# Performance work log

Measured on AMD Instinct MI355X. Metric: run time of the kernel, lower is better.

The kernel has to match this reference:

```python
import jax, jax.numpy as jnp
import numpy as np

_EPS = 1e-5
_NH, _DH = 4, 64  # heads, dim_head


def _ln(x, g, b):
    m = x.mean(-1, keepdims=True)
    v = ((x - m) ** 2).mean(-1, keepdims=True)
    return (x - m) / jnp.sqrt(v + _EPS) * g + b


def _leaky(x):
    return jnp.where(x > 0, x, 0.01 * x)


def _bn_eval(x, g, b):
    # eval-mode BatchNorm with running_mean=0, running_var=1
    return x * (g / np.sqrt(1.0 + _EPS)) + b


def setup_inputs() -> dict:
    key = jax.random.key(0)
    ks = jax.random.split(key, 20)
    B, L, S, D, T, H = 4096, 8, 877, 256, 137, 128
    f = jnp.float32

    def rn(k, shape, s=0.02):
        return jax.random.normal(k, shape, dtype=f) * s

    inp = {}
    inp['source'] = jax.random.normal(ks[0], (B, S), dtype=f)
    inp['source_neighbor'] = jax.random.normal(ks[1], (B, L, S), dtype=f)
    inp['cell_inf'] = jax.random.uniform(ks[2], (B, L + 1, 13), dtype=f)
    # encoder_rna: 877 -> 512 -> 256, Linear+BN(eval)+LeakyReLU
    inp['enc_w1'] = rn(ks[3], (S, 512)); inp['enc_b1'] = jnp.zeros((512,), f)
    inp['enc_bn1_g'] = jnp.ones((512,), f); inp['enc_bn1_b'] = jnp.zeros((512,), f)
    inp['enc_w2'] = rn(ks[4], (512, D)); inp['enc_b2'] = jnp.zeros((D,), f)
    inp['enc_bn2_g'] = jnp.ones((D,), f); inp['enc_bn2_b'] = jnp.zeros((D,), f)
    # projection_rna: Linear(256,256) + LayerNorm + ReLU
    inp['proj_w'] = rn(ks[5], (D, D)); inp['proj_b'] = jnp.zeros((D,), f)
    inp['proj_ln_g'] = jnp.ones((D,), f); inp['proj_ln_b'] = jnp.zeros((D,), f)
    # 1-layer pre-norm transformer (4 heads, dim_head 64, ff_mult 2)
    inp['attn_ln_g'] = jnp.ones((D,), f); inp['attn_ln_b'] = jnp.zeros((D,), f)
    inp['wq'] = rn(ks[6], (D, D)); inp['wk'] = rn(ks[7], (D, D)); inp['wv'] = rn(ks[8], (D, D))
    inp['wo'] = rn(ks[9], (D, D)); inp['wo_b'] = jnp.zeros((D,), f)
    inp['ff_ln_g'] = jnp.ones((D,), f); inp['ff_ln_b'] = jnp.zeros((D,), f)
    inp['ff_w1'] = rn(ks[10], (D, 2 * D)); inp['ff_b1'] = jnp.zeros((2 * D,), f)
    inp['ff_w2'] = rn(ks[11], (2 * D, D)); inp['ff_b2'] = jnp.zeros((D,), f)
    # learned tokens
    inp['token_center'] = rn(ks[12], (1, 1, D))
    inp['token_neigh_1'] = rn(ks[13], (1, 1, D))
    inp['token_neigh_2'] = rn(ks[14], (1, 1, D))
    inp['cell_tokens'] = rn(ks[15], (1, 1, 13, D))
    # 137 independent predict heads, batched: Linear(256,128)+BN+LeakyReLU+Linear(128,1,no bias)
    inp['pred_w1'] = rn(ks[16], (T, D, H)); inp['pred_b1'] = jnp.zeros((T, H), f)
    inp['pred_bn_g'] = jnp.ones((T, H), f); inp['pred_bn_b'] = jnp.zeros((T, H), f)
    inp['pred_w2'] = rn(ks[17], (T, H))
    return inp


def _forward(source, source_neighbor, cell_inf, enc_w1, enc_b1, enc_bn1_g, enc_bn1_b,
             enc_w2, enc_b2, enc_bn2_g, enc_bn2_b, proj_w, proj_b, proj_ln_g, proj_ln_b,
             attn_ln_g, attn_ln_b, wq, wk, wv, wo, wo_b, ff_ln_g, ff_ln_b,
             ff_w1, ff_b1, ff_w2, ff_b2, token_center, token_neigh_1, token_neigh_2,
             cell_tokens, pred_w1, pred_b1, pred_bn_g, pred_bn_b, pred_w2):
    B = source.shape[0]
    x = jnp.concatenate([source[:, None, :], source_neighbor], axis=1)  # [B,N,877]
    N = x.shape[1]
    l = N - 1
    half = l // 2
    valid = jnp.abs(x).sum(-1) > 0                      # [B,N] bool
    vm = valid.astype(x.dtype)[..., None]               # [B,N,1]
    D = token_center.shape[-1]
    # role tokens: center / first-half neigh / second-half neigh, masked
    role = jnp.concatenate([
        token_center,
        jnp.broadcast_to(token_neigh_1, (1, half, D)),
        jnp.broadcast_to(token_neigh_2, (1, l - half, D)),
    ], axis=1) * vm                                      # [B,N,D]
    # class tokens: weighted sum over 13 cell-type tokens, masked
    class_tok = (cell_tokens * cell_inf[..., None]).sum(-2) * vm  # [B,N,D]
    # encoder_rna (dropouts are eval identity)
    h = _leaky(_bn_eval(x @ enc_w1 + enc_b1, enc_bn1_g, enc_bn1_b))
    h = _leaky(_bn_eval(h @ enc_w2 + enc_b2, enc_bn2_g, enc_bn2_b))  # [B,N,D]
    fo = h + role + class_tok
    fo = jax.nn.relu(_ln(fo @ proj_w + proj_b, proj_ln_g, proj_ln_b))
    # local graph transformer encoder (depth=1, pre-norm, masked attention)
    hn = _ln(fo, attn_ln_g, attn_ln_b)
    q = (hn @ wq).reshape(B, N, _NH, _DH)
    k = (hn @ wk).reshape(B, N, _NH, _DH)
    v = (hn @ wv).reshape(B, N, _NH, _DH)
    scores = jnp.einsum('bihd,bjhd->bhij', q, k) * (_DH ** -0.5)
    scores = jnp.where(valid[:, None, None, :], scores, -1e9)
    attn = jax.nn.softmax(scores, axis=-1)
    o = jnp.einsum('bhij,bjhd->bihd', attn, v).reshape(B, N, _NH * _DH)
    fo = fo + o @ wo + wo_b
    hn2 = _ln(fo, ff_ln_g, ff_ln_b)
    fo = fo + jax.nn.gelu(hn2 @ ff_w1 + ff_b1) @ ff_w2 + ff_b2
    feat = fo[:, 0, :]                                   # [B,D] center token
    # 137 predict heads as one batched GEMM + fused BN/LeakyReLU
    ph = jnp.einsum('bd,tdh->bth', feat, pred_w1) + pred_b1   # [B,137,128]
    ph = _leaky(_bn_eval(ph, pred_bn_g, pred_bn_b))
    out = jnp.einsum('bth,th->bt', ph, pred_w2)               # [B,137]
    return out


def reference(source, source_neighbor, cell_inf, enc_w1, enc_b1, enc_bn1_g, enc_bn1_b,
              enc_w2, enc_b2, enc_bn2_g, enc_bn2_b, proj_w, proj_b, proj_ln_g, proj_ln_b,
              attn_ln_g, attn_ln_b, wq, wk, wv, wo, wo_b, ff_ln_g, ff_ln_b,
              ff_w1, ff_b1, ff_w2, ff_b2, token_center, token_neigh_1, token_neigh_2,
              cell_tokens, pred_w1, pred_b1, pred_bn_g, pred_bn_b, pred_w2):
    return _forward(source, source_neighbor, cell_inf, enc_w1, enc_b1, enc_bn1_g, enc_bn1_b,
                    enc_w2, enc_b2, enc_bn2_g, enc_bn2_b, proj_w, proj_b, proj_ln_g, proj_ln_b,
                    attn_ln_g, attn_ln_b, wq, wk, wv, wo, wo_b, ff_ln_g, ff_ln_b,
                    ff_w1, ff_b1, ff_w2, ff_b2, token_center, token_neigh_1, token_neigh_2,
                    cell_tokens, pred_w1, pred_b1, pred_bn_g, pred_bn_b, pred_w2)
```

## Files before the change

### kernel.cpp

```cpp
#include <hip/hip_runtime.h>
#include <hip/hip_bf16.h>
#include <math.h>

typedef __hip_bfloat16 bf16;
typedef __attribute__((ext_vector_type(8))) short short8;
typedef __attribute__((ext_vector_type(4))) float f32x4;

#define BB 4096
#define LL 8
#define NN 9
#define SS 877
#define DD 256
#define D2 512
#define TT 137
#define HH 128
#define MM (BB*NN)
#define KP1 896

__device__ __forceinline__ float lrelu(float x){ return x > 0.f ? x : 0.01f*x; }
__device__ __forceinline__ float gelu_tanh(float x){
    float x3 = x*x*x;
    float t = tanhf(0.7978845608028654f*(x + 0.044715f*x3));
    return 0.5f*x*(1.f + t);
}
__device__ __forceinline__ short f2b(float x){
    union { bf16 h; short s; } u; u.h = __float2bfloat16(x); return u.s;
}
__device__ __forceinline__ float b2f(bf16 v){ return __bfloat162float(v); }

struct SwzD { const float* src; unsigned short* dst; int K; int N; int NB; long long base; };
struct SwzTab { SwzD d[10]; long long total; };

__global__ __launch_bounds__(256) void k_swzall(SwzTab tab){
    for (long long f0 = (long long)blockIdx.x*256 + threadIdx.x; f0 < tab.total;
         f0 += (long long)gridDim.x*256){
        int di = 0;
        #pragma unroll
        for (int q = 1; q < 10; q++) if (f0 >= tab.d[q].base) di = q;
        const SwzD dd = tab.d[di];
        long long f = f0 - dd.base;
        int j = (int)(f & 7); int lane = (int)((f>>3)&63); int h = (int)((f>>9)&7);
        long long u = f>>12;
        int nb = (int)(u % dd.NB), kb = (int)(u / dd.NB);
        int k = kb*32 + ((lane>>4)<<3) + j;
        int n = nb*128 + h*16 + (lane&15);
        float v = (k < dd.K) ? dd.src[(size_t)k*dd.N + n] : 0.f;
        dd.dst[f] = (unsigned short)f2b(v);
    }
}

__global__ __launch_bounds__(256) void k_prep(const float* __restrict__ src,
                                              const float* __restrict__ srcn,
                                              float* __restrict__ vm,
                                              unsigned short* __restrict__ xbf){
    int m = blockIdx.x; int b = m / NN, n = m % NN;
    const float* row = (n == 0) ? src + (size_t)b*SS
                                : srcn + ((size_t)b*LL + (n-1))*SS;
    unsigned short* orow = xbf + (size_t)m*KP1;
    float s = 0.f;
    for (int i = threadIdx.x; i < KP1; i += 256){
        float v = (i < SS) ? row[i] : 0.f;
        s += fabsf(v);
        orow[i] = (unsigned short)f2b(v);
    }
    #pragma unroll
    for (int o = 32; o > 0; o >>= 1) s += __shfl_xor(s, o);
    __shared__ float part[4];
    if ((threadIdx.x & 63) == 0) part[threadIdx.x>>6] = s;
    __syncthreads();
    if (threadIdx.x == 0)
        vm[m] = ((part[0]+part[1]+part[2]+part[3]) > 0.f) ? 1.f : 0.f;
}

#define EPI_NONE 0
#define EPI_BN_LEAKY 1
#define EPI_RES 2
#define EPI_GELU 3

__global__ __launch_bounds__(256) void k_mgemm(
    const unsigned short* __restrict__ A, int lda,
    const unsigned short* __restrict__ Wsw, int NB, int nKb,
    const float* __restrict__ bias, const float* __restrict__ bng,
    const float* __restrict__ bnb, const float* __restrict__ res,
    int res_stride, int mode,
    float* __restrict__ out, bf16* __restrict__ outbf, int ldo)
{
    __shared__ short8 As[512];
    int row0 = blockIdx.x*128;
    int nb = blockIdx.y;
    int tid = threadIdx.x;
    int wv = tid>>6, lane = tid&63;
    int wr = wv>>1, wc = wv&1;
    int quad = lane>>4, l15 = lane&15;

    f32x4 zz = {0.f,0.f,0.f,0.f};
    f32x4 acc[4][4];
    #pragma unroll
    for (int i=0;i<4;i++){ acc[i][0]=zz; acc[i][1]=zz; acc[i][2]=zz; acc[i][3]=zz; }

    int m0 = tid>>2, k8 = tid&3;
    int m1 = m0 + 64;
    int dst0 = (m0>>4)*64 + (m0&15) + (k8<<4);
    int dst1 = (m1>>4)*64 + (m1&15) + (k8<<4);
    const short8* W8 = (const short8*)Wsw;

    for (int kb = 0; kb < nKb; kb++){
        int k0 = kb*32;
        uint4 v0 = *(const uint4*)(A + (size_t)(row0+m0)*lda + k0 + k8*8);
        uint4 v1 = *(const uint4*)(A + (size_t)(row0+m1)*lda + k0 + k8*8);
        short8 bfr[4];
        #pragma unroll
        for (int h = 0; h < 4; h++)
            bfr[h] = W8[((size_t)(kb*NB + nb)*8 + wc*4 + h)*64 + lane];
        __syncthreads();
        ((uint4*)As)[dst0] = v0;
        ((uint4*)As)[dst1] = v1;
        __syncthreads();
        #pragma unroll
        for (int i = 0; i < 4; i++){
            short8 af = As[(wr*4+i)*64 + lane];
            #pragma unroll
            for (int h = 0; h < 4; h++)
                acc[i][h] = __builtin_amdgcn_mfma_f32_16x16x32_bf16(af, bfr[h], acc[i][h], 0,0,0);
        }
    }

    const float inv = rsqrtf(1.f + 1e-5f);
    #pragma unroll
    for (int i = 0; i < 4; i++){
        int rbase = row0 + wr*64 + i*16 + quad*4;
        #pragma unroll
        for (int h = 0; h < 4; h++){
            int c = nb*128 + wc*64 + h*16 + l15;
            float bi = bias ? bias[c] : 0.f;
            #pragma unroll
            for (int reg = 0; reg < 4; reg++){
                int r = rbase + reg;
                float y = acc[i][h][reg] + bi;
                if (mode == EPI_BN_LEAKY)      y = lrelu(y*(bng[c]*inv) + bnb[c]);
                else if (mode == EPI_RES)      y += res[(size_t)r*res_stride + c];
                else if (mode == EPI_GELU)     y = gelu_tanh(y);
                if (out)   out[(size_t)r*ldo + c] = y;
                if (outbf) outbf[(size_t)r*ldo + c] = __float2bfloat16(y);
            }
        }
    }
}

__global__ __launch_bounds__(256) void k_pred_mfma(
    const unsigned short* __restrict__ feat,
    const unsigned short* __restrict__ Wsw,
    const float* __restrict__ b1, const float* __restrict__ bg,
    const float* __restrict__ bb, const float* __restrict__ w2,
    float* __restrict__ outp)
{
    __shared__ short8 As[512];
    int row0 = blockIdx.x*128;
    int t = blockIdx.y;
    int tid = threadIdx.x;
    int wv = tid>>6, lane = tid&63;
    int quad = lane>>4, l15 = lane&15;

    const float inv = rsqrtf(1.f + 1e-5f);
    float b1v[8], bgv[8], bbv[8], w2v[8];
    #pragma unroll
    for (int h = 0; h < 8; h++){
        int hc = t*HH + h*16 + l15;
        b1v[h] = b1[hc]; bgv[h] = bg[hc]*inv; bbv[h] = bb[hc]; w2v[h] = w2[hc];
    }

    f32x4 zz = {0.f,0.f,0.f,0.f};
    f32x4 acc[2][8];
    #pragma unroll
    for (int i=0;i<2;i++)
        #pragma unroll
        for (int h=0;h<8;h++) acc[i][h] = zz;

    int m0 = tid>>2, k8 = tid&3;
    int m1 = m0 + 64;
    int dst0 = (m0>>4)*64 + (m0&15) + (k8<<4);
    int dst1 = (m1>>4)*64 + (m1&15) + (k8<<4);
    const short8* W8 = (const short8*)Wsw;

    for (int kb = 0; kb < 8; kb++){
        int k0 = kb*32;
        uint4 v0 = *(const uint4*)(feat + (size_t)(row0+m0)*DD + k0 + k8*8);
        uint4 v1 = *(const uint4*)(feat + (size_t)(row0+m1)*DD + k0 + k8*8);
        short8 bfr[8];
        #pragma unroll
        for (int h = 0; h < 8; h++)
            bfr[h] = W8[((size_t)(t*8 + kb)*8 + h)*64 + lane];
        __syncthreads();
        ((uint4*)As)[dst0] = v0;
        ((uint4*)As)[dst1] = v1;
        __syncthreads();
        #pragma unroll
        for (int i = 0; i < 2; i++){
            short8 af = As[(wv*2+i)*64 + lane];
            #pragma unroll
            for (int h = 0; h < 8; h++)
                acc[i][h] = __builtin_amdgcn_mfma_f32_16x16x32_bf16(af, bfr[h], acc[i][h], 0,0,0);
        }
    }

    #pragma unroll
    for (int i = 0; i < 2; i++){
        #pragma unroll
        for (int reg = 0; reg < 4; reg++){
            float p = 0.f;
            #pragma unroll
            for (int h = 0; h < 8; h++){
                float y = (acc[i][h][reg] + b1v[h])*bgv[h] + bbv[h];
                p += lrelu(y) * w2v[h];
            }
            p += __shfl_xor(p, 1);
            p += __shfl_xor(p, 2);
            p += __shfl_xor(p, 4);
            p += __shfl_xor(p, 8);
            if (l15 == 0){
                int r = row0 + wv*32 + i*16 + quad*4 + reg;
                outp[(size_t)r*TT + t] = p;
            }
        }
    }
}

__global__ __launch_bounds__(256) void k_rolecls(const float* __restrict__ tokc,
                                                 const float* __restrict__ tokn1,
                                                 const float* __restrict__ tokn2,
                                                 const float* __restrict__ cell_tokens,
                                                 const float* __restrict__ cell_inf,
                                                 const float* __restrict__ vm,
                                                 float* __restrict__ fo,
                                                 bf16* __restrict__ fobf){
    int m = blockIdx.x, d = threadIdx.x;
    int n = m % NN;
    float v = vm[m];
    const float* role = (n == 0) ? tokc : (n <= 4 ? tokn1 : tokn2);
    float cl = 0.f;
    #pragma unroll
    for (int c = 0; c < 13; c++)
        cl += cell_inf[(size_t)m*13 + c] * cell_tokens[c*DD + d];
    float y = fo[(size_t)m*DD + d] + (role[d] + cl) * v;
    fo[(size_t)m*DD + d] = y;
    fobf[(size_t)m*DD + d] = __float2bfloat16(y);
}

__device__ __forceinline__ float blksum(float v, float* part){
    #pragma unroll
    for (int o = 32; o > 0; o >>= 1) v += __shfl_xor(v, o);
    __syncthreads();
    if ((threadIdx.x & 63) == 0) part[threadIdx.x>>6] = v;
    __syncthreads();
    return part[0]+part[1]+part[2]+part[3];
}

__global__ __launch_bounds__(256) void k_lnchain(const float* __restrict__ in,
                                                 const float* __restrict__ g1, const float* __restrict__ b1,
                                                 const float* __restrict__ g2, const float* __restrict__ b2,
                                                 float* __restrict__ fo1, bf16* __restrict__ hn){
    __shared__ float part[4];
    int m = blockIdx.x, d = threadIdx.x;
    float x = in[(size_t)m*DD + d];
    float mu = blksum(x, part) * (1.f/256.f);
    float dx = x - mu;
    float var = blksum(dx*dx, part) * (1.f/256.f);
    float y = dx * rsqrtf(var + 1e-5f) * g1[d] + b1[d];
    y = fmaxf(y, 0.f);
    fo1[(size_t)m*DD + d] = y;
    float mu2 = blksum(y, part) * (1.f/256.f);
    float dy = y - mu2;
    float var2 = blksum(dy*dy, part) * (1.f/256.f);
    hn[(size_t)m*DD + d] = __float2bfloat16(dy * rsqrtf(var2 + 1e-5f) * g2[d] + b2[d]);
}

__global__ __launch_bounds__(256) void k_ln(const float* __restrict__ in,
                                            const float* __restrict__ g, const float* __restrict__ b,
                                            bf16* __restrict__ out){
    __shared__ float part[4];
    int m = blockIdx.x, d = threadIdx.x;
    float x = in[(size_t)m*DD + d];
    float mu = blksum(x, part) * (1.f/256.f);
    float dx = x - mu;
    float var = blksum(dx*dx, part) * (1.f/256.f);
    out[(size_t)m*DD + d] = __float2bfloat16(dx * rsqrtf(var + 1e-5f) * g[d] + b[d]);
}

__global__ __launch_bounds__(256) void k_attn(const bf16* __restrict__ q,
                                              const bf16* __restrict__ k,
                                              const bf16* __restrict__ v,
                                              const float* __restrict__ vm,
                                              bf16* __restrict__ o){
    int b = blockIdx.x, t = threadIdx.x;
    __shared__ float ks[NN][DD];
    __shared__ float vs[NN][DD];
    __shared__ float qs[DD];
    __shared__ float sc[4][NN];
    __shared__ float val[NN];
    qs[t] = b2f(q[(size_t)b*DD + t]);
    for (int j = 0; j < NN; j++){
        ks[j][t] = b2f(k[((size_t)b*NN + j)*DD + t]);
        vs[j][t] = b2f(v[((size_t)b*NN + j)*DD + t]);
    }
    if (t < NN) val[t] = vm[b*NN + t];
    __syncthreads();
    if (t < 4*NN){
        int h = t / NN, j = t % NN;
        float s = 0.f;
        for (int d = 0; d < 64; d++) s += qs[h*64+d] * ks[j][h*64+d];
        s *= 0.125f;
        if (!(val[j] > 0.f)) s = -1e9f;
        sc[h][j] = s;
    }
    __syncthreads();
    if (t < 4){
        float mx = -1e30f;
        for (int j = 0; j < NN; j++) mx = fmaxf(mx, sc[t][j]);
        float den = 0.f;
        for (int j = 0; j < NN; j++){ float e = expf(sc[t][j]-mx); sc[t][j] = e; den += e; }
        float iv = 1.f/den;
        for (int j = 0; j < NN; j++) sc[t][j] *= iv;
    }
    __syncthreads();
    int h = t >> 6;
    float acc = 0.f;
    for (int j = 0; j < NN; j++) acc += sc[h][j] * vs[j][t];
    o[(size_t)b*DD + t] = __float2bfloat16(acc);
}

extern "C" void kernel_launch(void* const* d_in, const int* in_sizes, int n_in,
                              void* d_out, int out_size, void* d_ws, size_t ws_size,
                              hipStream_t stream) {
    const float* src      = (const float*)d_in[0];
    const float* srcn     = (const float*)d_in[1];
    const float* cell_inf = (const float*)d_in[2];
    const float* enc_w1   = (const float*)d_in[3];
    const float* enc_b1   = (const float*)d_in[4];
    const float* bn1g     = (const float*)d_in[5];
    const float* bn1b     = (const float*)d_in[6];
    const float* enc_w2   = (const float*)d_in[7];
    const float* enc_b2   = (const float*)d_in[8];
    const float* bn2g     = (const float*)d_in[9];
    const float* bn2b     = (const float*)d_in[10];
    const float* proj_w   = (const float*)d_in[11];
    const float* proj_b   = (const float*)d_in[12];
    const float* pln_g    = (const float*)d_in[13];
    const float* pln_b    = (const float*)d_in[14];
    const float* aln_g    = (const float*)d_in[15];
    const float* aln_b    = (const float*)d_in[16];
    const float* wq       = (const float*)d_in[17];
    const float* wk       = (const float*)d_in[18];
    const float* wv       = (const float*)d_in[19];
    const float* wo       = (const float*)d_in[20];
    const float* wo_b     = (const float*)d_in[21];
    const float* fln_g    = (const float*)d_in[22];
    const float* fln_b    = (const float*)d_in[23];
    const float* ff_w1    = (const float*)d_in[24];
    const float* ff_b1    = (const float*)d_in[25];
    const float* ff_w2    = (const float*)d_in[26];
    const float* ff_b2    = (const float*)d_in[27];
    const float* tokc     = (const float*)d_in[28];
    const float* tokn1    = (const float*)d_in[29];
    const float* tokn2    = (const float*)d_in[30];
    const float* cell_tok = (const float*)d_in[31];
    const float* pw1      = (const float*)d_in[32];
    const float* pb1      = (const float*)d_in[33];
    const float* pbg      = (const float*)d_in[34];
    const float* pbb      = (const float*)d_in[35];
    const float* pw2      = (const float*)d_in[36];
    float* out            = (float*)d_out;

    char* base = (char*)d_ws;
    size_t off = 0;
    auto alloc = [&](size_t bytes)->char*{
        char* p = base + off;
        off += (bytes + 255) & ~(size_t)255;
        return p;
    };
    bf16* sw_enc1 = (bf16*)alloc((size_t)KP1*D2*2);
    bf16* sw_enc2 = (bf16*)alloc((size_t)D2*DD*2);
    bf16* sw_proj = (bf16*)alloc((size_t)DD*DD*2);
    bf16* sw_wq   = (bf16*)alloc((size_t)DD*DD*2);
    bf16* sw_wk   = (bf16*)alloc((size_t)DD*DD*2);
    bf16* sw_wv   = (bf16*)alloc((size_t)DD*DD*2);
    bf16* sw_wo   = (bf16*)alloc((size_t)DD*DD*2);
    bf16* sw_ff1  = (bf16*)alloc((size_t)DD*D2*2);
    bf16* sw_ff2  = (bf16*)alloc((size_t)D2*DD*2);
    bf16* sw_pred = (bf16*)alloc((size_t)TT*DD*HH*2);
    float* vm    = (float*)alloc((size_t)MM*4);
    char*  xreg  = alloc((size_t)MM*KP1*2);
    bf16*  h1bf  = (bf16*)alloc((size_t)MM*D2*2);
    float* t0    = (float*)alloc((size_t)MM*DD*4);
    bf16*  hnbf  = (bf16*)alloc((size_t)MM*DD*2);
    bf16*  qbf   = (bf16*)alloc((size_t)BB*DD*2);
    bf16*  obbf  = (bf16*)alloc((size_t)BB*DD*2);
    float* fo2   = (float*)alloc((size_t)BB*DD*4);
    bf16*  hn2bf = (bf16*)alloc((size_t)BB*DD*2);
    bf16*  g1bf  = (bf16*)alloc((size_t)BB*D2*2);
    bf16*  featbf= (bf16*)alloc((size_t)BB*DD*2);
    unsigned short* xbf = (unsigned short*)xreg;
    float* fo   = (float*)xreg;
    bf16*  fobf = (bf16*)(xreg + (size_t)MM*DD*4);
    bf16* kbbf = h1bf;
    bf16* vbbf = h1bf + (size_t)MM*DD;

    dim3 blk(256);

    SwzTab tab;
    long long cum = 0;
    auto mk = [&](int slot, const float* s, bf16* d, int K, int Kpad, int N, int NB){
        tab.d[slot] = SwzD{ s, (unsigned short*)d, K, N, NB, cum };
        cum += (long long)Kpad*N;
    };
    mk(0, enc_w1, sw_enc1, SS, KP1, D2, 4);
    mk(1, enc_w2, sw_enc2, D2, D2, DD, 2);
    mk(2, proj_w, sw_proj, DD, DD, DD, 2);
    mk(3, wq,     sw_wq,   DD, DD, DD, 2);
    mk(4, wk,     sw_wk,   DD, DD, DD, 2);
    mk(5, wv,     sw_wv,   DD, DD, DD, 2);
    mk(6, wo,     sw_wo,   DD, DD, DD, 2);
    mk(7, ff_w1,  sw_ff1,  DD, DD, D2, 4);
    mk(8, ff_w2,  sw_ff2,  D2, D2, DD, 2);
    mk(9, pw1,    sw_pred, TT*DD, TT*DD, HH, 1);
    tab.total = cum;
    k_swzall<<<1024, blk, 0, stream>>>(tab);

    k_prep<<<MM, blk, 0, stream>>>(src, srcn, vm, xbf);

    k_mgemm<<<dim3(MM/128, 4), blk, 0, stream>>>(xbf, KP1,
        (const unsigned short*)sw_enc1, 4, KP1/32, enc_b1, bn1g, bn1b,
        nullptr, 0, EPI_BN_LEAKY, nullptr, h1bf, D2);
    k_mgemm<<<dim3(MM/128, 2), blk, 0, stream>>>((const unsigned short*)h1bf, D2,
        (const unsigned short*)sw_enc2, 2, 16, enc_b2, bn2g, bn2b,
        nullptr, 0, EPI_BN_LEAKY, fo, nullptr, DD);
    k_rolecls<<<MM, blk, 0, stream>>>(tokc, tokn1, tokn2, cell_tok, cell_inf, vm, fo, fobf);
    k_mgemm<<<dim3(MM/128, 2), blk, 0, stream>>>((const unsigned short*)fobf, DD,
        (const unsigned short*)sw_proj, 2, 8, proj_b, nullptr, nullptr,
        nullptr, 0, EPI_NONE, t0, nullptr, DD);
    k_lnchain<<<MM, blk, 0, stream>>>(t0, pln_g, pln_b, aln_g, aln_b, fo, hnbf);
    k_mgemm<<<dim3(MM/128, 2), blk, 0, stream>>>((const unsigned short*)hnbf, DD,
        (const unsigned short*)sw_wk, 2, 8, nullptr, nullptr, nullptr,
        nullptr, 0, EPI_NONE, nullptr, kbbf, DD);
    k_mgemm<<<dim3(MM/128, 2), blk, 0, stream>>>((const unsigned short*)hnbf, DD,
        (const unsigned short*)sw_wv, 2, 8, nullptr, nullptr, nullptr,
        nullptr, 0, EPI_NONE, nullptr, vbbf, DD);
    k_mgemm<<<dim3(BB/128, 2), blk, 0, stream>>>((const unsigned short*)hnbf, NN*DD,
        (const unsigned short*)sw_wq, 2, 8, nullptr, nullptr, nullptr,
        nullptr, 0, EPI_NONE, nullptr, qbf, DD);
    k_attn<<<BB, blk, 0, stream>>>(qbf, kbbf, vbbf, vm, obbf);
    k_mgemm<<<dim3(BB/128, 2), blk, 0, stream>>>((const unsigned short*)obbf, DD,
        (const unsigned short*)sw_wo, 2, 8, wo_b, nullptr, nullptr,
        fo, NN*DD, EPI_RES, fo2, nullptr, DD);
    k_ln<<<BB, blk, 0, stream>>>(fo2, fln_g, fln_b, hn2bf);
    k_mgemm<<<dim3(BB/128, 4), blk, 0, stream>>>((const unsigned short*)hn2bf, DD,
        (const unsigned short*)sw_ff1, 4, 8, ff_b1, nullptr, nullptr,
        nullptr, 0, EPI_GELU, nullptr, g1bf, D2);
    k_mgemm<<<dim3(BB/128, 2), blk, 0, stream>>>((const unsigned short*)g1bf, D2,
        (const unsigned short*)sw_ff2, 2, 16, ff_b2, nullptr, nullptr,
        fo2, DD, EPI_RES, nullptr, featbf, DD);
    k_pred_mfma<<<dim3(BB/128, TT), blk, 0, stream>>>((const unsigned short*)featbf,
        (const unsigned short*)sw_pred, pb1, pbg, pbb, pw2, out);
}
```

Baseline: 757.8 us.

## Double-buffer GEMM LDS tiles with register prefetch and fuse K/V projections

The generic MFMA GEMM and the predict-head kernel now keep two LDS buffers and prefetch the next A and W tiles into registers. This needs one barrier per k-step instead of two, and global loads overlap with MFMA work. The separate K and V projection GEMMs are merged into one GEMM with a concatenated swizzled weight (N=512), and attention reads the interleaved KV buffer. The cost is higher register pressure from the prefetch registers, which may reduce occupancy.

```diff
diff --git a/kernel.cpp b/kernel.cpp
--- a/kernel.cpp
+++ b/kernel.cpp
@@ -28,7 +28,8 @@
 }
 __device__ __forceinline__ float b2f(bf16 v){ return __bfloat162float(v); }
 
-struct SwzD { const float* src; unsigned short* dst; int K; int N; int NB; long long base; };
+struct SwzD { const float* src; unsigned short* dst; int K; int Nloc; int NBloc;
+              int NBt; int nbOff; long long base; };
 struct SwzTab { SwzD d[10]; long long total; };
 
 __global__ __launch_bounds__(256) void k_swzall(SwzTab tab){
@@ -41,11 +42,12 @@
         long long f = f0 - dd.base;
         int j = (int)(f & 7); int lane = (int)((f>>3)&63); int h = (int)((f>>9)&7);
         long long u = f>>12;
-        int nb = (int)(u % dd.NB), kb = (int)(u / dd.NB);
+        int nbl = (int)(u % dd.NBloc), kb = (int)(u / dd.NBloc);
         int k = kb*32 + ((lane>>4)<<3) + j;
-        int n = nb*128 + h*16 + (lane&15);
-        float v = (k < dd.K) ? dd.src[(size_t)k*dd.N + n] : 0.f;
-        dd.dst[f] = (unsigned short)f2b(v);
+        int n = nbl*128 + h*16 + (lane&15);
+        float v = (k < dd.K) ? dd.src[(size_t)k*dd.Nloc + n] : 0.f;
+        size_t dsti = ((((size_t)kb*dd.NBt + dd.nbOff + nbl)*8 + h)*64 + lane)*8 + j;
+        dd.dst[dsti] = (unsigned short)f2b(v);
     }
 }
 
@@ -79,19 +81,18 @@
 
 __global__ __launch_bounds__(256) void k_mgemm(
     const unsigned short* __restrict__ A, int lda,
-    const unsigned short* __restrict__ Wsw, int NB, int nKb,
+    const unsigned short* __restrict__ Wsw, int NBt, int nKb,
     const float* __restrict__ bias, const float* __restrict__ bng,
     const float* __restrict__ bnb, const float* __restrict__ res,
     int res_stride, int mode,
     float* __restrict__ out, bf16* __restrict__ outbf, int ldo)
 {
-    __shared__ short8 As[512];
+    __shared__ short8 As[2][8][64];
     int row0 = blockIdx.x*128;
     int nb = blockIdx.y;
     int tid = threadIdx.x;
     int wv = tid>>6, lane = tid&63;
-    int wr = wv>>1, wc = wv&1;
-    int quad = lane>>4, l15 = lane&15;
+    int wr = wv>>1, wc = wv&1, quad = lane>>4, l15 = lane&15;
 
     f32x4 zz = {0.f,0.f,0.f,0.f};
     f32x4 acc[4][4];
@@ -99,29 +100,49 @@
     for (int i=0;i<4;i++){ acc[i][0]=zz; acc[i][1]=zz; acc[i][2]=zz; acc[i][3]=zz; }
 
     int m0 = tid>>2, k8 = tid&3;
-    int m1 = m0 + 64;
     int dst0 = (m0>>4)*64 + (m0&15) + (k8<<4);
-    int dst1 = (m1>>4)*64 + (m1&15) + (k8<<4);
+    int dst1 = dst0 + 256;
+    const uint4* A0p = (const uint4*)(A + (size_t)(row0+m0)*lda + k8*8);
+    const uint4* A1p = (const uint4*)(A + (size_t)(row0+m0+64)*lda + k8*8);
+    int ldau4 = lda >> 3;
+    (void)ldau4;
     const short8* W8 = (const short8*)Wsw;
 
+    uint4 a1r0, a1r1, a2r0, a2r1;
+    short8 w[4], nw[4];
+
+    {
+        uint4 x0 = A0p[0], x1 = A1p[0];
+        ((uint4*)As[0])[dst0] = x0;
+        ((uint4*)As[0])[dst1] = x1;
+        a1r0 = A0p[4]; a1r1 = A1p[4];
+        #pragma unroll
+        for (int h = 0; h < 4; h++)
+            w[h] = W8[((size_t)nb*8 + wc*4 + h)*64 + lane];
+    }
     for (int kb = 0; kb < nKb; kb++){
-        int k0 = kb*32;
-        uint4 v0 = *(const uint4*)(A + (size_t)(row0+m0)*lda + k0 + k8*8);
-        uint4 v1 = *(const uint4*)(A + (size_t)(row0+m1)*lda + k0 + k8*8);
-        short8 bfr[4];
-        #pragma unroll
-        for (int h = 0; h < 4; h++)
-            bfr[h] = W8[((size_t)(kb*NB + nb)*8 + wc*4 + h)*64 + lane];
+        int buf = kb & 1;
+        if (kb+2 < nKb){ a2r0 = A0p[(kb+2)*4]; a2r1 = A1p[(kb+2)*4]; }
+        if (kb+1 < nKb){
+            #pragma unroll
+            for (int h = 0; h < 4; h++)
+                nw[h] = W8[((size_t)((kb+1)*NBt + nb)*8 + wc*4 + h)*64 + lane];
+        }
         __syncthreads();
-        ((uint4*)As)[dst0] = v0;
-        ((uint4*)As)[dst1] = v1;
-        __syncthreads();
-        #pragma unroll
-        for (int i = 0; i < 4; i++){
-            short8 af = As[(wr*4+i)*64 + lane];
+        short8 afr[4];
+        #pragma unroll
+        for (int i = 0; i < 4; i++) afr[i] = As[buf][wr*4+i][lane];
+        #pragma unroll
+        for (int i = 0; i < 4; i++)
             #pragma unroll
             for (int h = 0; h < 4; h++)
-                acc[i][h] = __builtin_amdgcn_mfma_f32_16x16x32_bf16(af, bfr[h], acc[i][h], 0,0,0);
+                acc[i][h] = __builtin_amdgcn_mfma_f32_16x16x32_bf16(afr[i], w[h], acc[i][h], 0,0,0);
+        if (kb+1 < nKb){
+            ((uint4*)As[buf^1])[dst0] = a1r0;
+            ((uint4*)As[buf^1])[dst1] = a1r1;
+            a1r0 = a2r0; a1r1 = a2r1;
+            #pragma unroll
+            for (int h = 0; h < 4; h++) w[h] = nw[h];
         }
     }
 
@@ -147,14 +168,14 @@
     }
 }
 
-__global__ __launch_bounds__(256) void k_pred_mfma(
+__global__ __launch_bounds__(256) void k_pred(
     const unsigned short* __restrict__ feat,
     const unsigned short* __restrict__ Wsw,
     const float* __restrict__ b1, const float* __restrict__ bg,
     const float* __restrict__ bb, const float* __restrict__ w2,
     float* __restrict__ outp)
 {
-    __shared__ short8 As[512];
+    __shared__ short8 As[2][8][64];
     int row0 = blockIdx.x*128;
     int t = blockIdx.y;
     int tid = threadIdx.x;
@@ -177,29 +198,46 @@
         for (int h=0;h<8;h++) acc[i][h] = zz;
 
     int m0 = tid>>2, k8 = tid&3;
-    int m1 = m0 + 64;
     int dst0 = (m0>>4)*64 + (m0&15) + (k8<<4);
-    int dst1 = (m1>>4)*64 + (m1&15) + (k8<<4);
+    int dst1 = dst0 + 256;
+    const uint4* A0p = (const uint4*)(feat + (size_t)(row0+m0)*DD + k8*8);
+    const uint4* A1p = (const uint4*)(feat + (size_t)(row0+m0+64)*DD + k8*8);
     const short8* W8 = (const short8*)Wsw;
 
+    uint4 a1r0, a1r1, a2r0, a2r1;
+    short8 w[8], nw[8];
+    {
+        uint4 x0 = A0p[0], x1 = A1p[0];
+        ((uint4*)As[0])[dst0] = x0;
+        ((uint4*)As[0])[dst1] = x1;
+        a1r0 = A0p[4]; a1r1 = A1p[4];
+        #pragma unroll
+        for (int h = 0; h < 8; h++)
+            w[h] = W8[((size_t)(t*8)*8 + h)*64 + lane];
+    }
     for (int kb = 0; kb < 8; kb++){
-        int k0 = kb*32;
-        uint4 v0 = *(const uint4*)(feat + (size_t)(row0+m0)*DD + k0 + k8*8);
-        uint4 v1 = *(const uint4*)(feat + (size_t)(row0+m1)*DD + k0 + k8*8);
-        short8 bfr[8];
-        #pragma unroll
-        for (int h = 0; h < 8; h++)
-            bfr[h] = W8[((size_t)(t*8 + kb)*8 + h)*64 + lane];
+        int buf = kb & 1;
+        if (kb+2 < 8){ a2r0 = A0p[(kb+2)*4]; a2r1 = A1p[(kb+2)*4]; }
+        if (kb+1 < 8){
+            #pragma unroll
+            for (int h = 0; h < 8; h++)
+                nw[h] = W8[((size_t)(t*8 + kb+1)*8 + h)*64 + lane];
+        }
         __syncthreads();
-        ((uint4*)As)[dst0] = v0;
-        ((uint4*)As)[dst1] = v1;
-        __syncthreads();
-        #pragma unroll
-        for (int i = 0; i < 2; i++){
-            short8 af = As[(wv*2+i)*64 + lane];
+        short8 afr[2];
+        #pragma unroll
+        for (int i = 0; i < 2; i++) afr[i] = As[buf][wv*2+i][lane];
+        #pragma unroll
+        for (int i = 0; i < 2; i++)
             #pragma unroll
             for (int h = 0; h < 8; h++)
-                acc[i][h] = __builtin_amdgcn_mfma_f32_16x16x32_bf16(af, bfr[h], acc[i][h], 0,0,0);
+                acc[i][h] = __builtin_amdgcn_mfma_f32_16x16x32_bf16(afr[i], w[h], acc[i][h], 0,0,0);
+        if (kb+1 < 8){
+            ((uint4*)As[buf^1])[dst0] = a1r0;
+            ((uint4*)As[buf^1])[dst1] = a1r1;
+            a1r0 = a2r0; a1r1 = a2r1;
+            #pragma unroll
+            for (int h = 0; h < 8; h++) w[h] = nw[h];
         }
     }
 
@@ -287,8 +325,7 @@
 }
 
 __global__ __launch_bounds__(256) void k_attn(const bf16* __restrict__ q,
-                                              const bf16* __restrict__ k,
-                                              const bf16* __restrict__ v,
+                                              const bf16* __restrict__ kv,
                                               const float* __restrict__ vm,
                                               bf16* __restrict__ o){
     int b = blockIdx.x, t = threadIdx.x;
@@ -299,8 +336,8 @@
     __shared__ float val[NN];
     qs[t] = b2f(q[(size_t)b*DD + t]);
     for (int j = 0; j < NN; j++){
-        ks[j][t] = b2f(k[((size_t)b*NN + j)*DD + t]);
-        vs[j][t] = b2f(v[((size_t)b*NN + j)*DD + t]);
+        ks[j][t] = b2f(kv[((size_t)b*NN + j)*D2 + t]);
+        vs[j][t] = b2f(kv[((size_t)b*NN + j)*D2 + DD + t]);
     }
     if (t < NN) val[t] = vm[b*NN + t];
     __syncthreads();
@@ -381,8 +418,7 @@
     bf16* sw_enc2 = (bf16*)alloc((size_t)D2*DD*2);
     bf16* sw_proj = (bf16*)alloc((size_t)DD*DD*2);
     bf16* sw_wq   = (bf16*)alloc((size_t)DD*DD*2);
-    bf16* sw_wk   = (bf16*)alloc((size_t)DD*DD*2);
-    bf16* sw_wv   = (bf16*)alloc((size_t)DD*DD*2);
+    bf16* sw_kv   = (bf16*)alloc((size_t)DD*D2*2);
     bf16* sw_wo   = (bf16*)alloc((size_t)DD*DD*2);
     bf16* sw_ff1  = (bf16*)alloc((size_t)DD*D2*2);
     bf16* sw_ff2  = (bf16*)alloc((size_t)D2*DD*2);
@@ -401,27 +437,27 @@
     unsigned short* xbf = (unsigned short*)xreg;
     float* fo   = (float*)xreg;
     bf16*  fobf = (bf16*)(xreg + (size_t)MM*DD*4);
-    bf16* kbbf = h1bf;
-    bf16* vbbf = h1bf + (size_t)MM*DD;
+    bf16* kvbf  = h1bf;
 
     dim3 blk(256);
 
     SwzTab tab;
     long long cum = 0;
-    auto mk = [&](int slot, const float* s, bf16* d, int K, int Kpad, int N, int NB){
-        tab.d[slot] = SwzD{ s, (unsigned short*)d, K, N, NB, cum };
-        cum += (long long)Kpad*N;
+    auto mk = [&](int slot, const float* s, bf16* d, int K, int Kpad, int Nloc,
+                  int NBt, int nbOff){
+        tab.d[slot] = SwzD{ s, (unsigned short*)d, K, Nloc, Nloc/128, NBt, nbOff, cum };
+        cum += (long long)Kpad*Nloc;
     };
-    mk(0, enc_w1, sw_enc1, SS, KP1, D2, 4);
-    mk(1, enc_w2, sw_enc2, D2, D2, DD, 2);
-    mk(2, proj_w, sw_proj, DD, DD, DD, 2);
-    mk(3, wq,     sw_wq,   DD, DD, DD, 2);
-    mk(4, wk,     sw_wk,   DD, DD, DD, 2);
-    mk(5, wv,     sw_wv,   DD, DD, DD, 2);
-    mk(6, wo,     sw_wo,   DD, DD, DD, 2);
-    mk(7, ff_w1,  sw_ff1,  DD, DD, D2, 4);
-    mk(8, ff_w2,  sw_ff2,  D2, D2, DD, 2);
-    mk(9, pw1,    sw_pred, TT*DD, TT*DD, HH, 1);
+    mk(0, enc_w1, sw_enc1, SS, KP1, D2, 4, 0);
+    mk(1, enc_w2, sw_enc2, D2, D2, DD, 2, 0);
+    mk(2, proj_w, sw_proj, DD, DD, DD, 2, 0);
+    mk(3, wq,     sw_wq,   DD, DD, DD, 2, 0);
+    mk(4, wk,     sw_kv,   DD, DD, DD, 4, 0);
+    mk(5, wv,     sw_kv,   DD, DD, DD, 4, 2);
+    mk(6, wo,     sw_wo,   DD, DD, DD, 2, 0);
+    mk(7, ff_w1,  sw_ff1,  DD, DD, D2, 4, 0);
+    mk(8, ff_w2,  sw_ff2,  D2, D2, DD, 2, 0);
+    mk(9, pw1,    sw_pred, TT*DD, TT*DD, HH, 1, 0);
     tab.total = cum;
     k_swzall<<<1024, blk, 0, stream>>>(tab);
 
@@ -438,16 +474,13 @@
         (const unsigned short*)sw_proj, 2, 8, proj_b, nullptr, nullptr,
         nullptr, 0, EPI_NONE, t0, nullptr, DD);
     k_lnchain<<<MM, blk, 0, stream>>>(t0, pln_g, pln_b, aln_g, aln_b, fo, hnbf);
-    k_mgemm<<<dim3(MM/128, 2), blk, 0, stream>>>((const unsigned short*)hnbf, DD,
-        (const unsigned short*)sw_wk, 2, 8, nullptr, nullptr, nullptr,
-        nullptr, 0, EPI_NONE, nullptr, kbbf, DD);
-    k_mgemm<<<dim3(MM/128, 2), blk, 0, stream>>>((const unsigned short*)hnbf, DD,
-        (const unsigned short*)sw_wv, 2, 8, nullptr, nullptr, nullptr,
-        nullptr, 0, EPI_NONE, nullptr, vbbf, DD);
+    k_mgemm<<<dim3(MM/128, 4), blk, 0, stream>>>((const unsigned short*)hnbf, DD,
+        (const unsigned short*)sw_kv, 4, 8, nullptr, nullptr, nullptr,
+        nullptr, 0, EPI_NONE, nullptr, kvbf, D2);
     k_mgemm<<<dim3(BB/128, 2), blk, 0, stream>>>((const unsigned short*)hnbf, NN*DD,
         (const unsigned short*)sw_wq, 2, 8, nullptr, nullptr, nullptr,
         nullptr, 0, EPI_NONE, nullptr, qbf, DD);
-    k_attn<<<BB, blk, 0, stream>>>(qbf, kbbf, vbbf, vm, obbf);
+    k_attn<<<BB, blk, 0, stream>>>(qbf, kvbf, vm, obbf);
     k_mgemm<<<dim3(BB/128, 2), blk, 0, stream>>>((const unsigned short*)obbf, DD,
         (const unsigned short*)sw_wo, 2, 8, wo_b, nullptr, nullptr,
         fo, NN*DD, EPI_RES, fo2, nullptr, DD);
@@ -458,6 +491,6 @@
     k_mgemm<<<dim3(BB/128, 2), blk, 0, stream>>>((const unsigned short*)g1bf, D2,
         (const unsigned short*)sw_ff2, 2, 16, ff_b2, nullptr, nullptr,
         fo2, DD, EPI_RES, nullptr, featbf, DD);
-    k_pred_mfma<<<dim3(BB/128, TT), blk, 0, stream>>>((const unsigned short*)featbf,
+    k_pred<<<dim3(BB/128, TT), blk, 0, stream>>>((const unsigned short*)featbf,
         (const unsigned short*)sw_pred, pb1, pbg, pbb, pw2, out);
 }
```

New measurement: 780.6 us. 3.0% more time.
